# Optimization experiments

Hardware: AMD Instinct MI355X
Metric: run time of the kernel (lower is better)

Reference implementation:

```python
import jax, jax.numpy as jnp
import numpy as np


def setup_inputs() -> dict:
    key = jax.random.key(0)
    k1, k2, k3, k4 = jax.random.split(key, 4)
    B, c_in, N, L = 32, 64, 512, 64
    K, c_out = 3, 64
    x = jax.random.normal(k1, (B, c_in, N, L), dtype=jnp.float32)
    adj = jax.random.uniform(k2, (N, N), dtype=jnp.float32)
    ds = jax.random.uniform(k3, (B, N, N), dtype=jnp.float32)
    W = jax.random.normal(k4, (c_out, K * c_in), dtype=jnp.float32) * 0.02
    b = jnp.zeros((c_out,), dtype=jnp.float32)
    return {"x": x, "adj": adj, "ds": ds, "W": W, "b": b}


def reference(x, adj, ds, W, b):
    B, c_in, N, L = x.shape
    K = W.shape[1] // c_in
    I = jnp.eye(N, dtype=x.dtype)
    # Chebyshev polynomial recurrence T_k(adj), each scaled per-sample by ds
    Ls = [ds * I, ds * adj]          # each [B, N, N]
    L0, L1 = I, adj
    for _ in range(2, K):
        L2 = 2.0 * (adj @ L1) - L0
        L0, L1 = L1, L2
        Ls.append(ds * L2)
    Lap = jnp.stack(Ls, axis=1)      # [B, K, N, N]
    Lap = jnp.swapaxes(Lap, -1, -2)  # transpose(-1, -2)
    # bcnl, bknq -> bckql : contract over node axis n
    xk = jnp.einsum('bcnl,bknq->bckql', x, Lap)
    xk = xk.reshape(B, c_in * K, N, L)
    # 1x1 Conv2d == channel-mixing matmul
    out = jnp.einsum('bfnl,of->bonl', xk, W) + b[None, :, None, None]
    return out
```

## Files before the change

kernel.cpp:

```cpp
#include <hip/hip_runtime.h>
#include <stdint.h>

typedef __bf16 bf16x8 __attribute__((ext_vector_type(8)));
typedef float  f32x4  __attribute__((ext_vector_type(4)));

#define AS1 __attribute__((address_space(1)))
#define AS3 __attribute__((address_space(3)))

__device__ __forceinline__ void gload_lds16(const void* g, void* l) {
    __builtin_amdgcn_global_load_lds((const AS1 uint32_t*)g, (AS3 uint32_t*)l, 16, 0, 0);
}


__global__ __launch_bounds__(256) void k_t2(const float* __restrict__ adj,
                                            float* __restrict__ T2f) {
    const int q = blockIdx.x, tx = threadIdx.x;
    float a0 = 0.f, a1 = 0.f;
    for (int m = 0; m < 512; ++m) {
        const float av = adj[q*512 + m];
        a0 += av * adj[m*512 + tx];
        a1 += av * adj[m*512 + tx + 256];
    }
    T2f[q*512 + tx      ] = 2.f*a0 - ((q == tx      ) ? 1.f : 0.f);
    T2f[q*512 + tx + 256] = 2.f*a1 - ((q == tx + 256) ? 1.f : 0.f);
}

__global__ __launch_bounds__(256) void k_w2(const float* __restrict__ W,
                                            __bf16* __restrict__ W2bf) {
    const int t = blockIdx.x*256 + threadIdx.x;
    const int f = t >> 6, c = t & 63;
    const int k = f >> 6, o = f & 63;
    W2bf[t] = (__bf16)W[o*192 + c*3 + k];
}

__global__ __launch_bounds__(256) void k_abuild(const float* __restrict__ ds,
                                                const float* __restrict__ adj,
                                                const float* __restrict__ T2f,
                                                __bf16* __restrict__ Abf, int b0) {
    const int bx = blockIdx.x;
    const int bb = bx >> 9, q = bx & 511;
    const int b  = b0 + bb;
    const float* dsr  = ds  + ((size_t)b*512 + q)*512;
    __bf16*      arow = Abf + ((size_t)bb*512 + q)*1536;
    for (int j = threadIdx.x; j < 1536; j += 256) {
        const int k = j >> 9, n = j & 511;
        float tv;
        if      (k == 0) tv = (q == n) ? 1.0f : 0.0f;
        else if (k == 1) tv = adj[q*512 + n];
        else             tv = T2f[q*512 + n];
        arow[j] = (__bf16)(dsr[n] * tv);
    }
}

__global__ __launch_bounds__(256) void k_zprep(const float* __restrict__ x,
                                               const __bf16* __restrict__ W2bf,
                                               __bf16* __restrict__ zT, int b0) {
    __shared__ __align__(16) char lds_raw[52224];
    __bf16* W2s = (__bf16*)lds_raw;
    __bf16* Xs  = (__bf16*)(lds_raw + 27648);
    __bf16* Dsh = (__bf16*)lds_raw;

    const int t = threadIdx.x, lane = t & 63, w = t >> 6;
    const int nb = gridDim.x;
    int bx = blockIdx.x;
    bx = (bx & 7) * (nb >> 3) + (bx >> 3);
    const int bb = bx >> 8;  const int r = bx & 255;
    const int ng = r >> 4, lg = r & 15;
    const int l0 = lg*4, n0 = ng*32;
    const int b  = b0 + bb;

    #pragma unroll
    for (int i = 0; i < 6; ++i) {
        const int u = t + 256*i, f = u >> 3, seg = u & 7;
        *(bf16x8*)(W2s + f*72 + seg*8) = *(const bf16x8*)(W2bf + f*64 + seg*8);
    }
    #pragma unroll
    for (int p = 0; p < 8; ++p) {
        const int u = t + 256*p, c = u >> 5, nn = u & 31;
        const float4 v = *(const float4*)(x + (((size_t)b*64 + c)*512 + (n0 + nn))*64 + l0);
        Xs[(nn     )*72 + c] = (__bf16)v.x;
        Xs[(nn + 32)*72 + c] = (__bf16)v.y;
        Xs[(nn + 64)*72 + c] = (__bf16)v.z;
        Xs[(nn + 96)*72 + c] = (__bf16)v.w;
    }
    __syncthreads();

    f32x4 acc[3][8] = {};
    const int fw = w*48, m15 = lane & 15, quad = lane >> 4;
    #pragma unroll
    for (int ks = 0; ks < 2; ++ks) {
        const int c0 = ks*32 + quad*8;
        bf16x8 a[3], bv[8];
        #pragma unroll
        for (int i = 0; i < 3; ++i)
            a[i] = *(const bf16x8*)(W2s + (fw + i*16 + m15)*72 + c0);
        #pragma unroll
        for (int j = 0; j < 8; ++j)
            bv[j] = *(const bf16x8*)(Xs + (j*16 + m15)*72 + c0);
        #pragma unroll
        for (int i = 0; i < 3; ++i)
            #pragma unroll
            for (int j = 0; j < 8; ++j)
                acc[i][j] = __builtin_amdgcn_mfma_f32_16x16x32_bf16(a[i], bv[j], acc[i][j], 0, 0, 0);
    }
    __syncthreads();

    #pragma unroll
    for (int i = 0; i < 3; ++i)
        #pragma unroll
        for (int j = 0; j < 8; ++j) {
            const int f = fw + i*16 + quad*4, m = j*16 + m15;
            #pragma unroll
            for (int rr = 0; rr < 4; ++rr)
                Dsh[(f + rr)*136 + m] = (__bf16)acc[i][j][rr];
        }
    __syncthreads();

    #pragma unroll
    for (int i = 0; i < 3; ++i) {
        const int u = t + 256*i, f = u >> 2, lp = u & 3;
        const int k = f >> 6, o = f & 63;
        __bf16* dst = zT + ((size_t)bb*4096 + o*64 + (l0 + lp))*1536 + k*512 + n0;
        const __bf16* srcp = Dsh + f*136 + lp*32;
        *(bf16x8*)(dst +  0) = *(const bf16x8*)(srcp +  0);
        *(bf16x8*)(dst +  8) = *(const bf16x8*)(srcp +  8);
        *(bf16x8*)(dst + 16) = *(const bf16x8*)(srcp + 16);
        *(bf16x8*)(dst + 24) = *(const bf16x8*)(srcp + 24);
    }
}

__global__ __launch_bounds__(256) void k_gemm(const __bf16* __restrict__ Abf,
                                              const __bf16* __restrict__ zT,
                                              const float* __restrict__ bias,
                                              float* __restrict__ out, int b0) {
    __shared__ __align__(16) __bf16 As[128*32];
    __shared__ __align__(16) __bf16 Bs[128*32];
    const int t = threadIdx.x, lane = t & 63, w = t >> 6;
    const int nb = gridDim.x;
    int bx = blockIdx.x;
    bx = (bx & 7) * (nb >> 3) + (bx >> 3);
    const int bb = bx >> 7;  const int r = bx & 127;
    const int qt = r & 3, ft = r >> 2;
    const int q0 = qt*128, f20 = ft*128;
    const __bf16* Ab = Abf + (size_t)bb*512 *1536;
    const __bf16* Bb = zT  + (size_t)bb*4096*1536;
    const int lrow = lane >> 2, lseg = lane & 3;
    const int m15 = lane & 15, quad = lane >> 4;
    const int wq = (w >> 1)*64, wf = (w & 1)*64;

    f32x4 acc[4][4] = {};
    for (int j0 = 0; j0 < 1536; j0 += 32) {
        #pragma unroll
        for (int i = 0; i < 2; ++i) {
            const int rb = (w*2 + i)*16;
            gload_lds16(Ab + ((size_t)(q0  + rb + lrow))*1536 + j0 + lseg*8, As + rb*32);
            gload_lds16(Bb + ((size_t)(f20 + rb + lrow))*1536 + j0 + lseg*8, Bs + rb*32);
        }
        __syncthreads();
        bf16x8 av[4], bv[4];
        const int co = quad*8;
        #pragma unroll
        for (int i = 0; i < 4; ++i) av[i] = *(const bf16x8*)(As + (wq + i*16 + m15)*32 + co);
        #pragma unroll
        for (int j = 0; j < 4; ++j) bv[j] = *(const bf16x8*)(Bs + (wf + j*16 + m15)*32 + co);
        #pragma unroll
        for (int i = 0; i < 4; ++i)
            #pragma unroll
            for (int j = 0; j < 4; ++j)
                acc[i][j] = __builtin_amdgcn_mfma_f32_16x16x32_bf16(av[i], bv[j], acc[i][j], 0, 0, 0);
        __syncthreads();
    }

    const int b = b0 + bb;
    #pragma unroll
    for (int j = 0; j < 4; ++j) {
        const int f2 = f20 + wf + j*16 + m15;
        const int o = f2 >> 6, l = f2 & 63;
        const float bi = bias[o];
        #pragma unroll
        for (int i = 0; i < 4; ++i) {
            const int qb = q0 + wq + i*16 + quad*4;
            float* dst = out + (((size_t)b*64 + o)*512 + qb)*64 + l;
            dst[  0] = acc[i][j][0] + bi;
            dst[ 64] = acc[i][j][1] + bi;
            dst[128] = acc[i][j][2] + bi;
            dst[192] = acc[i][j][3] + bi;
        }
    }
}

extern "C" void kernel_launch(void* const* d_in, const int* in_sizes, int n_in,
                              void* d_out, int out_size, void* d_ws, size_t ws_size,
                              hipStream_t stream) {
    (void)in_sizes; (void)n_in; (void)out_size;
    const float* x    = (const float*)d_in[0];
    const float* adj  = (const float*)d_in[1];
    const float* ds   = (const float*)d_in[2];
    const float* W    = (const float*)d_in[3];
    const float* bias = (const float*)d_in[4];
    float* out = (float*)d_out;
    char*  ws  = (char*)d_ws;

    float*  T2f  = (float*)ws;
    __bf16* W2bf = (__bf16*)(ws + (1u << 20));
    char*   chunk0 = ws + (1u << 20) + 32768;

    const size_t abytes = (size_t)512 *1536*2;
    const size_t zbytes = (size_t)4096*1536*2;
    const size_t perb   = abytes + zbytes;
    const size_t head   = (1u << 20) + 32768;

    int bpc = 1;
    if (ws_size > head) {
        size_t a = (ws_size - head) / perb;
        bpc = (a < 1) ? 1 : (a > 32 ? 32 : (int)a);
    }

    k_t2<<<dim3(512), dim3(256), 0, stream>>>(adj, T2f);
    k_w2<<<dim3(48),  dim3(256), 0, stream>>>(W, W2bf);

    __bf16* Abf = (__bf16*)chunk0;
    __bf16* zTp = (__bf16*)(chunk0 + (size_t)bpc*abytes);
    for (int b0 = 0; b0 < 32; b0 += bpc) {
        const int bc = (32 - b0 < bpc) ? (32 - b0) : bpc;
        k_abuild<<<dim3(bc*512), dim3(256), 0, stream>>>(ds, adj, T2f, Abf, b0);
        k_zprep <<<dim3(bc*256), dim3(256), 0, stream>>>(x, W2bf, zTp, b0);
        k_gemm  <<<dim3(bc*128), dim3(256), 0, stream>>>(Abf, zTp, bias, out, b0);
    }
}
```

Baseline: 983.5 us.

## Skip identity Chebyshev block in GEMM and double-buffer LDS tiles

```diff
diff --git a/kernel.cpp b/kernel.cpp
--- a/kernel.cpp
+++ b/kernel.cpp
@@ -9,6 +9,10 @@
 
 __device__ __forceinline__ void gload_lds16(const void* g, void* l) {
     __builtin_amdgcn_global_load_lds((const AS1 uint32_t*)g, (AS3 uint32_t*)l, 16, 0, 0);
+}
+
+__device__ __forceinline__ float bf2f(unsigned short u) {
+    union { unsigned int i; float f; } v; v.i = ((unsigned int)u) << 16; return v.f;
 }
 
 
@@ -36,18 +40,17 @@
 __global__ __launch_bounds__(256) void k_abuild(const float* __restrict__ ds,
                                                 const float* __restrict__ adj,
                                                 const float* __restrict__ T2f,
-                                                __bf16* __restrict__ Abf, int b0) {
+                                                __bf16* __restrict__ Abf,
+                                                float* __restrict__ dsd, int b0) {
     const int bx = blockIdx.x;
     const int bb = bx >> 9, q = bx & 511;
     const int b  = b0 + bb;
     const float* dsr  = ds  + ((size_t)b*512 + q)*512;
-    __bf16*      arow = Abf + ((size_t)bb*512 + q)*1536;
-    for (int j = threadIdx.x; j < 1536; j += 256) {
-        const int k = j >> 9, n = j & 511;
-        float tv;
-        if      (k == 0) tv = (q == n) ? 1.0f : 0.0f;
-        else if (k == 1) tv = adj[q*512 + n];
-        else             tv = T2f[q*512 + n];
+    __bf16*      arow = Abf + ((size_t)bb*512 + q)*1024;
+    if (threadIdx.x == 0) dsd[bb*512 + q] = dsr[q];
+    for (int j = threadIdx.x; j < 1024; j += 256) {
+        const int n = j & 511;
+        const float tv = (j < 512) ? adj[q*512 + n] : T2f[q*512 + n];
         arow[j] = (__bf16)(dsr[n] * tv);
     }
 }
@@ -131,10 +134,11 @@
 
 __global__ __launch_bounds__(256) void k_gemm(const __bf16* __restrict__ Abf,
                                               const __bf16* __restrict__ zT,
+                                              const float* __restrict__ dsd,
                                               const float* __restrict__ bias,
                                               float* __restrict__ out, int b0) {
-    __shared__ __align__(16) __bf16 As[128*32];
-    __shared__ __align__(16) __bf16 Bs[128*32];
+    __shared__ __align__(16) __bf16 As[2][128*32];
+    __shared__ __align__(16) __bf16 Bs[2][128*32];
     const int t = threadIdx.x, lane = t & 63, w = t >> 6;
     const int nb = gridDim.x;
     int bx = blockIdx.x;
@@ -142,33 +146,63 @@
     const int bb = bx >> 7;  const int r = bx & 127;
     const int qt = r & 3, ft = r >> 2;
     const int q0 = qt*128, f20 = ft*128;
-    const __bf16* Ab = Abf + (size_t)bb*512 *1536;
+    const __bf16* Ab = Abf + (size_t)bb*512 *1024;
     const __bf16* Bb = zT  + (size_t)bb*4096*1536;
     const int lrow = lane >> 2, lseg = lane & 3;
     const int m15 = lane & 15, quad = lane >> 4;
     const int wq = (w >> 1)*64, wf = (w & 1)*64;
+    const int rb0 = w*32;
 
     f32x4 acc[4][4] = {};
-    for (int j0 = 0; j0 < 1536; j0 += 32) {
+
+    auto stage = [&](int buf, int it) {
+        const int j0 = it * 32;
         #pragma unroll
         for (int i = 0; i < 2; ++i) {
-            const int rb = (w*2 + i)*16;
-            gload_lds16(Ab + ((size_t)(q0  + rb + lrow))*1536 + j0 + lseg*8, As + rb*32);
-            gload_lds16(Bb + ((size_t)(f20 + rb + lrow))*1536 + j0 + lseg*8, Bs + rb*32);
-        }
-        __syncthreads();
+            const int rb = rb0 + i*16;
+            gload_lds16(Ab + (size_t)(q0  + rb + lrow)*1024 + j0       + lseg*8, &As[buf][rb*32]);
+            gload_lds16(Bb + (size_t)(f20 + rb + lrow)*1536 + 512 + j0 + lseg*8, &Bs[buf][rb*32]);
+        }
+    };
+    auto compute = [&](int buf) {
         bf16x8 av[4], bv[4];
         const int co = quad*8;
         #pragma unroll
-        for (int i = 0; i < 4; ++i) av[i] = *(const bf16x8*)(As + (wq + i*16 + m15)*32 + co);
-        #pragma unroll
-        for (int j = 0; j < 4; ++j) bv[j] = *(const bf16x8*)(Bs + (wf + j*16 + m15)*32 + co);
+        for (int i = 0; i < 4; ++i) av[i] = *(const bf16x8*)(&As[buf][(wq + i*16 + m15)*32 + co]);
+        #pragma unroll
+        for (int j = 0; j < 4; ++j) bv[j] = *(const bf16x8*)(&Bs[buf][(wf + j*16 + m15)*32 + co]);
         #pragma unroll
         for (int i = 0; i < 4; ++i)
             #pragma unroll
             for (int j = 0; j < 4; ++j)
                 acc[i][j] = __builtin_amdgcn_mfma_f32_16x16x32_bf16(av[i], bv[j], acc[i][j], 0, 0, 0);
+    };
+
+    stage(0, 0);
+    __syncthreads();
+    int cur = 0;
+    for (int it = 0; it < 31; ++it) {
+        stage(cur ^ 1, it + 1);
+        compute(cur);
         __syncthreads();
+        cur ^= 1;
+    }
+    compute(cur);
+
+    const float* dsdb = dsd + bb*512;
+    #pragma unroll
+    for (int i = 0; i < 4; ++i) {
+        const int qb = q0 + wq + i*16 + quad*4;
+        const float4 dv = *(const float4*)(dsdb + qb);
+        #pragma unroll
+        for (int j = 0; j < 4; ++j) {
+            const int f2 = f20 + wf + j*16 + m15;
+            const ushort4 zv = *(const ushort4*)((const unsigned short*)Bb + (size_t)f2*1536 + qb);
+            acc[i][j][0] += dv.x * bf2f(zv.x);
+            acc[i][j][1] += dv.y * bf2f(zv.y);
+            acc[i][j][2] += dv.z * bf2f(zv.z);
+            acc[i][j][3] += dv.w * bf2f(zv.w);
+        }
     }
 
     const int b = b0 + bb;
@@ -203,12 +237,13 @@
 
     float*  T2f  = (float*)ws;
     __bf16* W2bf = (__bf16*)(ws + (1u << 20));
-    char*   chunk0 = ws + (1u << 20) + 32768;
-
-    const size_t abytes = (size_t)512 *1536*2;
+    float*  dsd  = (float*)(ws + (1u << 20) + 32768);
+    char*   chunk0 = ws + (1u << 20) + 32768 + 65536;
+
+    const size_t abytes = (size_t)512 *1024*2;
     const size_t zbytes = (size_t)4096*1536*2;
     const size_t perb   = abytes + zbytes;
-    const size_t head   = (1u << 20) + 32768;
+    const size_t head   = (1u << 20) + 32768 + 65536;
 
     int bpc = 1;
     if (ws_size > head) {
@@ -223,8 +258,8 @@
     __bf16* zTp = (__bf16*)(chunk0 + (size_t)bpc*abytes);
     for (int b0 = 0; b0 < 32; b0 += bpc) {
         const int bc = (32 - b0 < bpc) ? (32 - b0) : bpc;
-        k_abuild<<<dim3(bc*512), dim3(256), 0, stream>>>(ds, adj, T2f, Abf, b0);
+        k_abuild<<<dim3(bc*512), dim3(256), 0, stream>>>(ds, adj, T2f, Abf, dsd, b0);
         k_zprep <<<dim3(bc*256), dim3(256), 0, stream>>>(x, W2bf, zTp, b0);
-        k_gemm  <<<dim3(bc*128), dim3(256), 0, stream>>>(Abf, zTp, bias, out, b0);
-    }
-}
+        k_gemm  <<<dim3(bc*128), dim3(256), 0, stream>>>(Abf, zTp, dsd, bias, out, b0);
+    }
+}
```

Measured after the change: 944.7 us. -3.9%, faster.
